# Performance work log

Measured on AMD Instinct MI355X. Metric: run time of the kernel, lower is better.

The kernel has to match this reference:

```python
import jax, jax.numpy as jnp
import numpy as np

CUTOFF = 5.0
NUM_RADIAL = 8
MAX_DEGREE = 3
EMB_DIM = 64
N_ELEM = 83
N_EDGES = 400000
NUM_LM = (MAX_DEGREE + 1) ** 2  # 16
# degree of each (l,m) slot: [0, 1,1,1, 2x5, 3x7]
DEG = jnp.asarray([0] + [1] * 3 + [2] * 5 + [3] * 7, dtype=jnp.int32)


def _spherical_harmonics(u):
    """Racah-normalized real spherical harmonics up to l=3 on unit vectors u (N,3).
    Cartesian order for l=1 (x, y, z), standard m=-l..l order otherwise. Returns (N,16)."""
    x, y, z = u[:, 0], u[:, 1], u[:, 2]
    x2, y2, z2 = x * x, y * y, z * z
    s3 = jnp.sqrt(3.0)
    s15 = jnp.sqrt(15.0)
    s5_8 = jnp.sqrt(5.0 / 8.0)
    s3_8 = jnp.sqrt(3.0 / 8.0)
    cols = [
        jnp.ones_like(x),                 # l=0
        x, y, z,                          # l=1 (Cartesian order)
        s3 * x * y,                       # l=2, m=-2
        s3 * y * z,                       # l=2, m=-1
        0.5 * (3.0 * z2 - 1.0),           # l=2, m=0
        s3 * x * z,                       # l=2, m=1
        0.5 * s3 * (x2 - y2),             # l=2, m=2
        s5_8 * y * (3.0 * x2 - y2),       # l=3, m=-3
        s15 * x * y * z,                  # l=3, m=-2
        s3_8 * y * (5.0 * z2 - 1.0),      # l=3, m=-1
        0.5 * z * (5.0 * z2 - 3.0),       # l=3, m=0
        s3_8 * x * (5.0 * z2 - 1.0),      # l=3, m=1
        0.5 * s15 * z * (x2 - y2),        # l=3, m=2
        s5_8 * x * (x2 - 3.0 * y2),       # l=3, m=3
    ]
    return jnp.stack(cols, axis=-1)


def setup_inputs() -> dict:
    key = jax.random.key(0)
    k1, k2, k3, k4, k5 = jax.random.split(key, 5)
    # displacements scaled so |r| spans [0, cutoff] realistically
    neighbour_displacements = jax.random.normal(k1, (N_EDGES, 3), dtype=jnp.float32) * 2.0
    Z_j = jax.random.randint(k2, (N_EDGES,), 0, N_ELEM, dtype=jnp.int32)
    emb_table = jax.random.normal(k3, (N_ELEM, EMB_DIM), dtype=jnp.float32)
    dense_w = jax.random.normal(k4, (EMB_DIM, NUM_RADIAL), dtype=jnp.float32) / jnp.sqrt(float(EMB_DIM))
    dense_b = jnp.zeros((NUM_RADIAL,), dtype=jnp.float32)
    tensor_w = jax.random.normal(k5, (MAX_DEGREE + 1, NUM_RADIAL), dtype=jnp.float32)  # one weight per path (0,l,l)
    return {
        "neighbour_displacements": neighbour_displacements,
        "Z_j": Z_j,
        "emb_table": emb_table,
        "dense_w": dense_w,
        "dense_b": dense_b,
        "tensor_w": tensor_w,
    }


def reference(neighbour_displacements, Z_j, emb_table, dense_w, dense_b, tensor_w):
    d = neighbour_displacements
    r = jnp.linalg.norm(d, axis=-1)                        # (N,)
    r_safe = jnp.where(r > 0.0, r, 1.0)
    u = d / r_safe[:, None]                                # unit vectors (N,3)
    Y = _spherical_harmonics(u)                            # (N,16)
    # sinc radial basis: jnp.sinc(k * r / cutoff), k = 1..num_radial
    k = jnp.arange(1, NUM_RADIAL + 1, dtype=jnp.float32)
    radial = jnp.sinc(r[:, None] * k / CUTOFF)             # (N,8)
    cut = jnp.where(r < CUTOFF, 0.5 * (jnp.cos(jnp.pi * r / CUTOFF) + 1.0), 0.0)
    rb = radial * cut[:, None]                             # (N,8)
    basis = Y[:, :, None] * rb[:, None, :]                 # (N,16,8)
    # species embedding -> dense transform to num_radial channels (scalar feature)
    t = emb_table[Z_j] @ dense_w + dense_b                 # (N,8)
    # CG tensor product: scalar (l=0) x basis (l) -> l, per-path learnable weight
    w_lm = tensor_w[DEG]                                   # (16,8)
    y = t[:, None, :] * basis * w_lm[None]                 # (N,16,8)
    # equivariant swish: y_lm * sigmoid(y_00) (= swish on scalar channel)
    gate = jax.nn.sigmoid(y[:, 0:1, :])
    return y * gate
```

## Files before the change

kernel.cpp:

```cpp
#include <hip/hip_runtime.h>
#include <math.h>

#define NUM_RADIAL 8
#define EMB_DIM    64
#define N_ELEM     83
#define TILE       256

__global__ void srb_precompute_t(const float* __restrict__ emb,
                                 const float* __restrict__ dw,
                                 const float* __restrict__ db,
                                 float* __restrict__ t_table) {
    int idx = blockIdx.x * blockDim.x + threadIdx.x;
    if (idx >= N_ELEM * NUM_RADIAL) return;
    int z = idx >> 3;
    int k = idx & 7;
    float acc = db[k];
    const float* e = emb + z * EMB_DIM;
    #pragma unroll 8
    for (int j = 0; j < EMB_DIM; ++j)
        acc += e[j] * dw[j * NUM_RADIAL + k];
    t_table[idx] = acc;
}

__global__ __launch_bounds__(256) void srb_main(
    const float* __restrict__ disp,
    const int*   __restrict__ Zj,
    const float* __restrict__ tw,
    const float* __restrict__ t_table,
    float*       __restrict__ out,
    int n_edges)
{
    __shared__ float Yl[TILE * 17];
    __shared__ float Gl[TILE * 33];

    const int tid = threadIdx.x;
    const int e   = blockIdx.x * TILE + tid;

    float w[4][NUM_RADIAL];
    #pragma unroll
    for (int l = 0; l < 4; ++l)
        #pragma unroll
        for (int k = 0; k < NUM_RADIAL; ++k)
            w[l][k] = tw[l * NUM_RADIAL + k];

    if (e < n_edges) {
        const float dx = disp[3 * e + 0];
        const float dy = disp[3 * e + 1];
        const float dz = disp[3 * e + 2];
        const float r2 = dx * dx + dy * dy + dz * dz;
        const float r  = sqrtf(r2);
        const float rinv = (r > 0.0f) ? (1.0f / r) : 0.0f;
        const float x = dx * rinv, y = dy * rinv, z = dz * rinv;
        const float x2 = x * x, y2 = y * y, z2 = z * z;

        const float s3   = 1.7320508075688772f;
        const float s15  = 3.8729833462074170f;
        const float s5_8 = 0.7905694150420949f;
        const float s3_8 = 0.6123724356957945f;

        float* Yp = &Yl[tid * 17];
        Yp[0]  = 1.0f;
        Yp[1]  = x;
        Yp[2]  = y;
        Yp[3]  = z;
        Yp[4]  = s3 * x * y;
        Yp[5]  = s3 * y * z;
        Yp[6]  = 0.5f * (3.0f * z2 - 1.0f);
        Yp[7]  = s3 * x * z;
        Yp[8]  = 0.5f * s3 * (x2 - y2);
        Yp[9]  = s5_8 * y * (3.0f * x2 - y2);
        Yp[10] = s15 * x * y * z;
        Yp[11] = s3_8 * y * (5.0f * z2 - 1.0f);
        Yp[12] = 0.5f * z * (5.0f * z2 - 3.0f);
        Yp[13] = s3_8 * x * (5.0f * z2 - 1.0f);
        Yp[14] = 0.5f * s15 * z * (x2 - y2);
        Yp[15] = s5_8 * x * (x2 - 3.0f * y2);

        const float PI = 3.14159265358979323846f;
        const float cut = (r < 5.0f) ? (0.5f * (cosf(PI * r * 0.2f) + 1.0f))
                                     : 0.0f;
        const float pib = PI * r * 0.2f;

        const int zidx = Zj[e];
        const float4 t0 = reinterpret_cast<const float4*>(t_table)[zidx * 2 + 0];
        const float4 t1 = reinterpret_cast<const float4*>(t_table)[zidx * 2 + 1];
        float t[NUM_RADIAL] = { t0.x, t0.y, t0.z, t0.w, t1.x, t1.y, t1.z, t1.w };

        float* Gp = &Gl[tid * 33];
        #pragma unroll
        for (int k = 0; k < NUM_RADIAL; ++k) {
            const float px = pib * (float)(k + 1);
            const float s  = (px != 0.0f) ? (sinf(px) / px) : 1.0f;
            const float rb = s * cut;
            const float c  = t[k] * rb;
            const float y0 = c * w[0][k];
            const float gate = 1.0f / (1.0f + expf(-y0));
            const float cg = c * gate;
            Gp[0  + k] = cg * w[0][k];
            Gp[8  + k] = cg * w[1][k];
            Gp[16 + k] = cg * w[2][k];
            Gp[24 + k] = cg * w[3][k];
        }
    }

    __syncthreads();

    const int totalF4 = n_edges * 32;
    const int baseF4  = blockIdx.x * (TILE * 32);
    float4* out4 = reinterpret_cast<float4*>(out);
    #pragma unroll
    for (int it = 0; it < 32; ++it) {
        const int lf = it * 256 + tid;
        const int f  = baseF4 + lf;
        if (f < totalF4) {
            const int el = lf >> 5;
            const int j  = lf & 31;
            const int lm = j >> 1;
            const int k0 = (j & 1) * 4;
            const int l  = (lm > 0) + (lm > 3) + (lm > 8);
            const float yv = Yl[el * 17 + lm];
            const int gb = el * 33 + l * 8 + k0;
            float4 o;
            o.x = yv * Gl[gb + 0];
            o.y = yv * Gl[gb + 1];
            o.z = yv * Gl[gb + 2];
            o.w = yv * Gl[gb + 3];
            out4[f] = o;
        }
    }
}

extern "C" void kernel_launch(void* const* d_in, const int* in_sizes, int n_in,
                              void* d_out, int out_size, void* d_ws, size_t ws_size,
                              hipStream_t stream) {
    const float* disp = (const float*)d_in[0];
    const int*   Zj   = (const int*)  d_in[1];
    const float* emb  = (const float*)d_in[2];
    const float* dw   = (const float*)d_in[3];
    const float* db   = (const float*)d_in[4];
    const float* tw   = (const float*)d_in[5];
    float* t_table = (float*)d_ws;
    float* out     = (float*)d_out;

    const int n = in_sizes[1];

    hipLaunchKernelGGL(srb_precompute_t, dim3(3), dim3(256), 0, stream,
                       emb, dw, db, t_table);

    const int nblocks = (n + TILE - 1) / TILE;
    hipLaunchKernelGGL(srb_main, dim3(nblocks), dim3(256), 0, stream,
                       disp, Zj, tw, t_table, out, n);
}
```

Measured before the change: 44.77 us.

## Split each edge across four threads with fast math and nontemporal vector stores

Shrinks the block tile from 256 edges to 64, with four threads per edge, so each thread computes only two of the eight radial channels and a single lane writes the spherical harmonics. It also switches to fast intrinsics (__sinf, __cosf, __expf), pads the gate table to a 36-float stride so it can be read as float4 from LDS, and writes output with nontemporal vector stores. The intent is to spread the transcendental work over more threads, cut per-thread registers and LDS, raise occupancy, and keep the write-once output from occupying cache. The cost is that the displacement load and norm are now computed redundantly by four threads, and the fast intrinsics lose some accuracy.

```diff
diff --git a/kernel.cpp b/kernel.cpp
--- a/kernel.cpp
+++ b/kernel.cpp
@@ -4,7 +4,10 @@
 #define NUM_RADIAL 8
 #define EMB_DIM    64
 #define N_ELEM     83
-#define TILE       256
+#define TILE       64
+
+typedef float f4 __attribute__((ext_vector_type(4)));
+typedef float f2 __attribute__((ext_vector_type(2)));
 
 __global__ void srb_precompute_t(const float* __restrict__ emb,
                                  const float* __restrict__ dw,
@@ -31,17 +34,12 @@
     int n_edges)
 {
     __shared__ float Yl[TILE * 17];
-    __shared__ float Gl[TILE * 33];
+    __shared__ float Gl[TILE * 36];
 
     const int tid = threadIdx.x;
-    const int e   = blockIdx.x * TILE + tid;
-
-    float w[4][NUM_RADIAL];
-    #pragma unroll
-    for (int l = 0; l < 4; ++l)
-        #pragma unroll
-        for (int k = 0; k < NUM_RADIAL; ++k)
-            w[l][k] = tw[l * NUM_RADIAL + k];
+    const int el  = tid >> 2;
+    const int sub = tid & 3;
+    const int e   = blockIdx.x * TILE + el;
 
     if (e < n_edges) {
         const float dx = disp[3 * e + 0];
@@ -53,53 +51,57 @@
         const float x = dx * rinv, y = dy * rinv, z = dz * rinv;
         const float x2 = x * x, y2 = y * y, z2 = z * z;
 
-        const float s3   = 1.7320508075688772f;
-        const float s15  = 3.8729833462074170f;
-        const float s5_8 = 0.7905694150420949f;
-        const float s3_8 = 0.6123724356957945f;
-
-        float* Yp = &Yl[tid * 17];
-        Yp[0]  = 1.0f;
-        Yp[1]  = x;
-        Yp[2]  = y;
-        Yp[3]  = z;
-        Yp[4]  = s3 * x * y;
-        Yp[5]  = s3 * y * z;
-        Yp[6]  = 0.5f * (3.0f * z2 - 1.0f);
-        Yp[7]  = s3 * x * z;
-        Yp[8]  = 0.5f * s3 * (x2 - y2);
-        Yp[9]  = s5_8 * y * (3.0f * x2 - y2);
-        Yp[10] = s15 * x * y * z;
-        Yp[11] = s3_8 * y * (5.0f * z2 - 1.0f);
-        Yp[12] = 0.5f * z * (5.0f * z2 - 3.0f);
-        Yp[13] = s3_8 * x * (5.0f * z2 - 1.0f);
-        Yp[14] = 0.5f * s15 * z * (x2 - y2);
-        Yp[15] = s5_8 * x * (x2 - 3.0f * y2);
-
         const float PI = 3.14159265358979323846f;
-        const float cut = (r < 5.0f) ? (0.5f * (cosf(PI * r * 0.2f) + 1.0f))
+        const float cut = (r < 5.0f) ? (0.5f * (__cosf(PI * r * 0.2f) + 1.0f))
                                      : 0.0f;
         const float pib = PI * r * 0.2f;
 
+        if (sub == 0) {
+            const float s3   = 1.7320508075688772f;
+            const float s15  = 3.8729833462074170f;
+            const float s5_8 = 0.7905694150420949f;
+            const float s3_8 = 0.6123724356957945f;
+            float* Yp = &Yl[el * 17];
+            Yp[0]  = 1.0f;
+            Yp[1]  = x;
+            Yp[2]  = y;
+            Yp[3]  = z;
+            Yp[4]  = s3 * x * y;
+            Yp[5]  = s3 * y * z;
+            Yp[6]  = 0.5f * (3.0f * z2 - 1.0f);
+            Yp[7]  = s3 * x * z;
+            Yp[8]  = 0.5f * s3 * (x2 - y2);
+            Yp[9]  = s5_8 * y * (3.0f * x2 - y2);
+            Yp[10] = s15 * x * y * z;
+            Yp[11] = s3_8 * y * (5.0f * z2 - 1.0f);
+            Yp[12] = 0.5f * z * (5.0f * z2 - 3.0f);
+            Yp[13] = s3_8 * x * (5.0f * z2 - 1.0f);
+            Yp[14] = 0.5f * s15 * z * (x2 - y2);
+            Yp[15] = s5_8 * x * (x2 - 3.0f * y2);
+        }
+
         const int zidx = Zj[e];
-        const float4 t0 = reinterpret_cast<const float4*>(t_table)[zidx * 2 + 0];
-        const float4 t1 = reinterpret_cast<const float4*>(t_table)[zidx * 2 + 1];
-        float t[NUM_RADIAL] = { t0.x, t0.y, t0.z, t0.w, t1.x, t1.y, t1.z, t1.w };
+        const f2 t2 = *reinterpret_cast<const f2*>(t_table + zidx * NUM_RADIAL + 2 * sub);
 
-        float* Gp = &Gl[tid * 33];
+        float cg[2];
         #pragma unroll
-        for (int k = 0; k < NUM_RADIAL; ++k) {
+        for (int kk = 0; kk < 2; ++kk) {
+            const int   k  = 2 * sub + kk;
             const float px = pib * (float)(k + 1);
-            const float s  = (px != 0.0f) ? (sinf(px) / px) : 1.0f;
+            const float s  = (px != 0.0f) ? (__sinf(px) / px) : 1.0f;
             const float rb = s * cut;
-            const float c  = t[k] * rb;
-            const float y0 = c * w[0][k];
-            const float gate = 1.0f / (1.0f + expf(-y0));
-            const float cg = c * gate;
-            Gp[0  + k] = cg * w[0][k];
-            Gp[8  + k] = cg * w[1][k];
-            Gp[16 + k] = cg * w[2][k];
-            Gp[24 + k] = cg * w[3][k];
+            const float c  = ((kk == 0) ? t2.x : t2.y) * rb;
+            const float y0 = c * tw[k];
+            const float gate = 1.0f / (1.0f + __expf(-y0));
+            cg[kk] = c * gate;
+        }
+        float* Gp = &Gl[el * 36 + 2 * sub];
+        #pragma unroll
+        for (int l = 0; l < 4; ++l) {
+            f2 v;
+            v.x = cg[0] * tw[l * NUM_RADIAL + 2 * sub + 0];
+            v.y = cg[1] * tw[l * NUM_RADIAL + 2 * sub + 1];
+            *reinterpret_cast<f2*>(&Gp[l * NUM_RADIAL]) = v;
         }
     }
 
@@ -107,25 +109,21 @@
 
     const int totalF4 = n_edges * 32;
     const int baseF4  = blockIdx.x * (TILE * 32);
-    float4* out4 = reinterpret_cast<float4*>(out);
+    f4* out4 = reinterpret_cast<f4*>(out);
     #pragma unroll
-    for (int it = 0; it < 32; ++it) {
+    for (int it = 0; it < 8; ++it) {
         const int lf = it * 256 + tid;
         const int f  = baseF4 + lf;
         if (f < totalF4) {
-            const int el = lf >> 5;
-            const int j  = lf & 31;
-            const int lm = j >> 1;
-            const int k0 = (j & 1) * 4;
-            const int l  = (lm > 0) + (lm > 3) + (lm > 8);
-            const float yv = Yl[el * 17 + lm];
-            const int gb = el * 33 + l * 8 + k0;
-            float4 o;
-            o.x = yv * Gl[gb + 0];
-            o.y = yv * Gl[gb + 1];
-            o.z = yv * Gl[gb + 2];
-            o.w = yv * Gl[gb + 3];
-            out4[f] = o;
+            const int el2 = lf >> 5;
+            const int j   = lf & 31;
+            const int lm  = j >> 1;
+            const int k0  = (j & 1) * 4;
+            const int l   = (lm > 0) + (lm > 3) + (lm > 8);
+            const float yv = Yl[el2 * 17 + lm];
+            const f4 g = *reinterpret_cast<const f4*>(&Gl[el2 * 36 + l * 8 + k0]);
+            const f4 o = yv * g;
+            __builtin_nontemporal_store(o, &out4[f]);
         }
     }
 }
```

New measurement: 48.55 us. 8.5% more time.

## Store gated radial coefficients once per edge and apply path weights at write-out

Applied to the files above, without the earlier changes.

Each thread now stores only the 8 gated coefficients per edge in shared memory, instead of 32 values premultiplied by each degree's weight. The per-lane weight vector is fixed because lane&31 determines lm, so it is loaded once and multiplied in the output loop. Shared-memory reads become single vector loads of 4 floats, and the write-out loop no longer recomputes its index math. Transcendental and division calls are also replaced with fast intrinsics (__sinf, __cosf, __expf, rcp), which trade some accuracy for fewer instructions.

```diff
diff --git a/kernel.cpp b/kernel.cpp
--- a/kernel.cpp
+++ b/kernel.cpp
@@ -5,6 +5,9 @@
 #define EMB_DIM    64
 #define N_ELEM     83
 #define TILE       256
+
+typedef float f4 __attribute__((ext_vector_type(4)));
+typedef float f2 __attribute__((ext_vector_type(2)));
 
 __global__ void srb_precompute_t(const float* __restrict__ emb,
                                  const float* __restrict__ dw,
@@ -31,17 +34,16 @@
     int n_edges)
 {
     __shared__ float Yl[TILE * 17];
-    __shared__ float Gl[TILE * 33];
+    __shared__ float CGl[TILE * 8];
 
     const int tid = threadIdx.x;
     const int e   = blockIdx.x * TILE + tid;
 
-    float w[4][NUM_RADIAL];
-    #pragma unroll
-    for (int l = 0; l < 4; ++l)
-        #pragma unroll
-        for (int k = 0; k < NUM_RADIAL; ++k)
-            w[l][k] = tw[l * NUM_RADIAL + k];
+    const int jj  = tid & 31;
+    const int lm  = jj >> 1;
+    const int k0  = (jj & 1) * 4;
+    const int l   = (lm > 0) + (lm > 3) + (lm > 8);
+    const f4  wl  = *reinterpret_cast<const f4*>(tw + l * NUM_RADIAL + k0);
 
     if (e < n_edges) {
         const float dx = disp[3 * e + 0];
@@ -49,7 +51,7 @@
         const float dz = disp[3 * e + 2];
         const float r2 = dx * dx + dy * dy + dz * dz;
         const float r  = sqrtf(r2);
-        const float rinv = (r > 0.0f) ? (1.0f / r) : 0.0f;
+        const float rinv = (r > 0.0f) ? __builtin_amdgcn_rcpf(r) : 0.0f;
         const float x = dx * rinv, y = dy * rinv, z = dz * rinv;
         const float x2 = x * x, y2 = y * y, z2 = z * z;
 
@@ -76,55 +78,47 @@
         Yp[14] = 0.5f * s15 * z * (x2 - y2);
         Yp[15] = s5_8 * x * (x2 - 3.0f * y2);
 
-        const float PI = 3.14159265358979323846f;
-        const float cut = (r < 5.0f) ? (0.5f * (cosf(PI * r * 0.2f) + 1.0f))
+        const float PI  = 3.14159265358979323846f;
+        const float cut = (r < 5.0f) ? (0.5f * (__cosf(PI * r * 0.2f) + 1.0f))
                                      : 0.0f;
         const float pib = PI * r * 0.2f;
 
         const int zidx = Zj[e];
-        const float4 t0 = reinterpret_cast<const float4*>(t_table)[zidx * 2 + 0];
-        const float4 t1 = reinterpret_cast<const float4*>(t_table)[zidx * 2 + 1];
+        const f4 t0 = *reinterpret_cast<const f4*>(t_table + zidx * NUM_RADIAL);
+        const f4 t1 = *reinterpret_cast<const f4*>(t_table + zidx * NUM_RADIAL + 4);
         float t[NUM_RADIAL] = { t0.x, t0.y, t0.z, t0.w, t1.x, t1.y, t1.z, t1.w };
 
-        float* Gp = &Gl[tid * 33];
+        f4 cga, cgb;
         #pragma unroll
         for (int k = 0; k < NUM_RADIAL; ++k) {
             const float px = pib * (float)(k + 1);
-            const float s  = (px != 0.0f) ? (sinf(px) / px) : 1.0f;
-            const float rb = s * cut;
-            const float c  = t[k] * rb;
-            const float y0 = c * w[0][k];
-            const float gate = 1.0f / (1.0f + expf(-y0));
+            const float s  = (px != 0.0f) ? (__sinf(px) * __builtin_amdgcn_rcpf(px))
+                                          : 1.0f;
+            const float c  = t[k] * (s * cut);
+            const float y0 = c * tw[k];
+            const float gate = __builtin_amdgcn_rcpf(1.0f + __expf(-y0));
             const float cg = c * gate;
-            Gp[0  + k] = cg * w[0][k];
-            Gp[8  + k] = cg * w[1][k];
-            Gp[16 + k] = cg * w[2][k];
-            Gp[24 + k] = cg * w[3][k];
+            if (k < 4) ((float*)&cga)[k] = cg; else ((float*)&cgb)[k - 4] = cg;
         }
+        f4* CGp = reinterpret_cast<f4*>(&CGl[tid * 8]);
+        CGp[0] = cga;
+        CGp[1] = cgb;
     }
 
     __syncthreads();
 
     const int totalF4 = n_edges * 32;
     const int baseF4  = blockIdx.x * (TILE * 32);
-    float4* out4 = reinterpret_cast<float4*>(out);
+    f4* out4 = reinterpret_cast<f4*>(out);
     #pragma unroll
     for (int it = 0; it < 32; ++it) {
         const int lf = it * 256 + tid;
         const int f  = baseF4 + lf;
         if (f < totalF4) {
             const int el = lf >> 5;
-            const int j  = lf & 31;
-            const int lm = j >> 1;
-            const int k0 = (j & 1) * 4;
-            const int l  = (lm > 0) + (lm > 3) + (lm > 8);
             const float yv = Yl[el * 17 + lm];
-            const int gb = el * 33 + l * 8 + k0;
-            float4 o;
-            o.x = yv * Gl[gb + 0];
-            o.y = yv * Gl[gb + 1];
-            o.z = yv * Gl[gb + 2];
-            o.w = yv * Gl[gb + 3];
+            const f4 cg = *reinterpret_cast<const f4*>(&CGl[el * 8 + k0]);
+            const f4 o  = (yv * cg) * wl;
             out4[f] = o;
         }
     }
```

Result: no change. 45.01 us (+0.5%).
